# Performance work log

Measured on AMD Instinct MI355X. Metric: run time of the kernel, lower is better.

## Reference

```python
import jax, jax.numpy as jnp
import numpy as np

B, E, F = 16384, 128, 6
ITEM_V, CATE_V, HIST = 91718, 11, 50
I_IDX, J_IDX = np.triu_indices(F, k=1)  # 15 field pairs, loop order (0,1),(0,2),...
EPS = 1e-5


def _xavier(key, shape):
    fan_in, fan_out = shape[0], shape[-1]
    std = (2.0 / (fan_in + fan_out)) ** 0.5
    return std * jax.random.normal(key, shape, dtype=jnp.float32)


def setup_inputs() -> dict:
    key = jax.random.key(0)
    ks = jax.random.split(key, 20)
    inp = {
        'item_id': jax.random.randint(ks[0], (B,), 0, ITEM_V),
        'item_emb_d128': jax.random.normal(ks[1], (B, 128), dtype=jnp.float32),
        'likes_level': jax.random.randint(ks[2], (B,), 0, CATE_V),
        'views_level': jax.random.randint(ks[3], (B,), 0, CATE_V),
        'item_seq': jax.random.randint(ks[4], (B, HIST), 0, ITEM_V),
        # learned parameters
        'item_emb': 0.05 * jax.random.normal(ks[5], (ITEM_V, E), dtype=jnp.float32),
        'cate_emb': 0.05 * jax.random.normal(ks[6], (CATE_V, E), dtype=jnp.float32),
        'mm_W': _xavier(ks[7], (128, E)), 'mm_b': jnp.zeros((E,), jnp.float32),
        'ln_g': jnp.ones((E,), jnp.float32), 'ln_b': jnp.zeros((E,), jnp.float32),
        'se_W1': _xavier(ks[8], (F, F // 2)), 'se_b1': jnp.zeros((F // 2,), jnp.float32),
        'se_W2': _xavier(ks[9], (F // 2, F)), 'se_b2': jnp.zeros((F,), jnp.float32),
        'bi_W': _xavier(ks[10], (E, E)),
        'mlp_W1': _xavier(ks[11], (21 * E, 512)), 'mlp_b1': jnp.zeros((512,), jnp.float32),
        'bn1_g': jnp.ones((512,), jnp.float32), 'bn1_b': jnp.zeros((512,), jnp.float32),
        'bn1_rm': jnp.zeros((512,), jnp.float32), 'bn1_rv': jnp.ones((512,), jnp.float32),
        'mlp_W2': _xavier(ks[12], (512, 256)), 'mlp_b2': jnp.zeros((256,), jnp.float32),
        'bn2_g': jnp.ones((256,), jnp.float32), 'bn2_b': jnp.zeros((256,), jnp.float32),
        'bn2_rm': jnp.zeros((256,), jnp.float32), 'bn2_rv': jnp.ones((256,), jnp.float32),
        'mlp_W3': _xavier(ks[13], (256, 1)), 'mlp_b3': jnp.zeros((1,), jnp.float32),
    }
    return inp


def _forward(item_id, item_emb_d128, likes_level, views_level, item_seq,
             item_emb, cate_emb, mm_W, mm_b, ln_g, ln_b,
             se_W1, se_b1, se_W2, se_b2, bi_W,
             mlp_W1, mlp_b1, bn1_g, bn1_b, bn1_rm, bn1_rv,
             mlp_W2, mlp_b2, bn2_g, bn2_b, bn2_rm, bn2_rv,
             mlp_W3, mlp_b3):
    b = item_id.shape[0]
    tab = item_emb.at[0].set(0.0)  # padding_idx=0
    like_feat = cate_emb[likes_level]
    view_feat = cate_emb[views_level]
    item_feat = tab[item_id]
    # mm_proj: Linear -> LayerNorm -> ReLU
    mm = item_emb_d128 @ mm_W + mm_b
    mu = mm.mean(-1, keepdims=True)
    var = jnp.var(mm, axis=-1, keepdims=True)
    mm = jax.nn.relu((mm - mu) / jnp.sqrt(var + EPS) * ln_g + ln_b)
    # masked mean pooling over history
    seq_emb = tab[item_seq]                               # (B, HIST, E)
    valid = (item_seq != 0).astype(seq_emb.dtype)
    seq_sum = (seq_emb * valid[..., None]).sum(1)
    cnt = jnp.clip(valid.sum(1, keepdims=True), 1.0)
    hist_feat = seq_sum / cnt
    user_feat = jnp.zeros((b, E), seq_emb.dtype)
    x = jnp.stack([user_feat, like_feat, view_feat, item_feat, mm, hist_feat], axis=1)  # (B,6,E)
    # SENet
    z = x.mean(-1)
    w = jax.nn.sigmoid(jax.nn.relu(z @ se_W1 + se_b1) @ se_W2 + se_b2)
    xs = x * w[:, :, None]
    # bilinear 'all'
    xw = jnp.einsum('bfe,ed->bfd', xs, bi_W)
    p = xs[:, I_IDX, :] * xw[:, J_IDX, :]                 # (B,15,E)
    c = jnp.concatenate([xs.reshape(b, -1), p.reshape(b, -1)], axis=1)  # (B, 2688)
    # MLP head (eval mode: BN uses running stats, dropout off)
    h = c @ mlp_W1 + mlp_b1
    h = jax.nn.relu((h - bn1_rm) / jnp.sqrt(bn1_rv + EPS) * bn1_g + bn1_b)
    h = h @ mlp_W2 + mlp_b2
    h = jax.nn.relu((h - bn2_rm) / jnp.sqrt(bn2_rv + EPS) * bn2_g + bn2_b)
    logits = h @ mlp_W3 + mlp_b3
    return jax.nn.sigmoid(logits)[:, 0]


def reference(item_id, item_emb_d128, likes_level, views_level, item_seq,
              item_emb, cate_emb, mm_W, mm_b, ln_g, ln_b,
              se_W1, se_b1, se_W2, se_b2, bi_W,
              mlp_W1, mlp_b1, bn1_g, bn1_b, bn1_rm, bn1_rv,
              mlp_W2, mlp_b2, bn2_g, bn2_b, bn2_rm, bn2_rv,
              mlp_W3, mlp_b3):
    return _forward(item_id, item_emb_d128, likes_level, views_level, item_seq,
                    item_emb, cate_emb, mm_W, mm_b, ln_g, ln_b,
                    se_W1, se_b1, se_W2, se_b2, bi_W,
                    mlp_W1, mlp_b1, bn1_g, bn1_b, bn1_rm, bn1_rv,
                    mlp_W2, mlp_b2, bn2_g, bn2_b, bn2_rm, bn2_rv,
                    mlp_W3, mlp_b3)
```

## Files before the change

kernel.cpp:

```cpp
#include <hip/hip_runtime.h>
#include <hip/hip_bf16.h>

typedef __hip_bfloat16 bfloat;
typedef __bf16 bf16x8 __attribute__((ext_vector_type(8)));
typedef float f32x4 __attribute__((ext_vector_type(4)));

#define B_SZ   16384
#define E_DIM  128
#define HIST_L 50


__device__ __constant__ int ISL[10] = {0,0,0,0,1,1,1,2,2,3};

__device__ __forceinline__ void gl_lds16(const void* g, void* l) {
    __builtin_amdgcn_global_load_lds(
        (const __attribute__((address_space(1))) unsigned int*)g,
        (__attribute__((address_space(3))) unsigned int*)l, 16, 0, 0);
}

template<int TB>
__global__ __launch_bounds__(256) void feat_kernel(
    const int* __restrict__ item_id,
    const int* __restrict__ likes, const int* __restrict__ views,
    const int* __restrict__ seq,
    const void* __restrict__ item_tab, const float* __restrict__ cate_emb,
    const float* __restrict__ mm,
    const float* __restrict__ ln_g, const float* __restrict__ ln_b,
    const float* __restrict__ se_W1, const float* __restrict__ se_b1,
    const float* __restrict__ se_W2, const float* __restrict__ se_b2,
    bfloat* __restrict__ xs)
{
    const int tid = threadIdx.x;
    const int r   = tid >> 7;
    const int e   = tid & 127;
    const int b   = blockIdx.x * 2 + r;
    const int w   = tid >> 6;

    __shared__ float redh[2][4][128];
    __shared__ int   seq_s[2][64];
    __shared__ float lnred[4], lnred2[4];
    __shared__ float zred[5][4];
    __shared__ float wsh[2][6];
    __shared__ int   cnt_s[2];

    if (e < 64) seq_s[r][e] = (e < HIST_L) ? seq[(size_t)b * HIST_L + e] : 0;
    __syncthreads();

    const int iid = item_id[b];
    const float like_v = cate_emb[likes[b] * 128 + e];
    const float view_v = cate_emb[views[b] * 128 + e];
    float item_v;
    if (TB) {
        const bfloat* tb = (const bfloat*)item_tab;
        item_v = __bfloat162float(tb[(size_t)iid * 128 + e]);
    } else {
        const float* tf = (const float*)item_tab;
        float raw = tf[(size_t)iid * 128 + e];
        item_v = iid ? raw : 0.f;
    }
    const float acc = mm[(size_t)b * 128 + e];

    const int q   = e >> 5;
    const int l32 = e & 31;
    float4 hs = make_float4(0.f, 0.f, 0.f, 0.f);
    if (TB) {
        const ushort* tb = (const ushort*)item_tab;
        #pragma unroll
        for (int g = 0; g < 13; ++g) {
            int s = seq_s[r][g * 4 + q];
            ushort4 v = *(const ushort4*)&tb[(size_t)s * 128 + l32 * 4];
            hs.x += __bfloat162float(__ushort_as_bfloat16(v.x));
            hs.y += __bfloat162float(__ushort_as_bfloat16(v.y));
            hs.z += __bfloat162float(__ushort_as_bfloat16(v.z));
            hs.w += __bfloat162float(__ushort_as_bfloat16(v.w));
        }
    } else {
        const float* tf = (const float*)item_tab;
        #pragma unroll
        for (int g = 0; g < 13; ++g) {
            int s = seq_s[r][g * 4 + q];
            const float4 v = *(const float4*)&tf[(size_t)s * 128 + l32 * 4];
            float m = (s != 0) ? 1.f : 0.f;
            hs.x = fmaf(v.x, m, hs.x);
            hs.y = fmaf(v.y, m, hs.y);
            hs.z = fmaf(v.z, m, hs.z);
            hs.w = fmaf(v.w, m, hs.w);
        }
    }

    {
        float v = acc;
        #pragma unroll
        for (int off = 32; off > 0; off >>= 1) v += __shfl_down(v, off, 64);
        if ((tid & 63) == 0) lnred[w] = v;
    }
    __syncthreads();
    const float mu = (lnred[2 * r] + lnred[2 * r + 1]) * (1.f / 128.f);
    const float d  = acc - mu;
    {
        float v = d * d;
        #pragma unroll
        for (int off = 32; off > 0; off >>= 1) v += __shfl_down(v, off, 64);
        if ((tid & 63) == 0) lnred2[w] = v;
    }
    redh[r][q][l32 * 4 + 0] = hs.x;
    redh[r][q][l32 * 4 + 1] = hs.y;
    redh[r][q][l32 * 4 + 2] = hs.z;
    redh[r][q][l32 * 4 + 3] = hs.w;
    if ((w & 1) == 0 && e < 64) {
        bool valid = (e < HIST_L) && (seq_s[r][e] != 0);
        unsigned long long m = __ballot(valid);
        if (e == 0) cnt_s[r] = (int)__popcll(m);
    }
    __syncthreads();
    const float var = (lnred2[2 * r] + lnred2[2 * r + 1]) * (1.f / 128.f);
    float xmm = d * rsqrtf(var + 1e-5f) * ln_g[e] + ln_b[e];
    xmm = fmaxf(xmm, 0.f);

    const int cnt = cnt_s[r] > 0 ? cnt_s[r] : 1;
    const float hist_v = (redh[r][0][e] + redh[r][1][e] +
                          redh[r][2][e] + redh[r][3][e]) / (float)cnt;

    {
        float s1 = like_v, s2 = view_v, s3 = item_v, s4 = xmm, s5 = hist_v;
        #pragma unroll
        for (int off = 32; off > 0; off >>= 1) {
            s1 += __shfl_down(s1, off, 64);
            s2 += __shfl_down(s2, off, 64);
            s3 += __shfl_down(s3, off, 64);
            s4 += __shfl_down(s4, off, 64);
            s5 += __shfl_down(s5, off, 64);
        }
        if ((tid & 63) == 0) {
            zred[0][w] = s1; zred[1][w] = s2; zred[2][w] = s3;
            zred[3][w] = s4; zred[4][w] = s5;
        }
    }
    __syncthreads();

    if (e == 0) {
        float z[6];
        z[0] = 0.f;
        #pragma unroll
        for (int f = 1; f < 6; ++f)
            z[f] = (zred[f - 1][2 * r] + zred[f - 1][2 * r + 1]) * (1.f / 128.f);
        float a[3];
        #pragma unroll
        for (int j = 0; j < 3; ++j) {
            float s = se_b1[j];
            #pragma unroll
            for (int f = 0; f < 6; ++f) s += z[f] * se_W1[f * 3 + j];
            a[j] = fmaxf(s, 0.f);
        }
        #pragma unroll
        for (int f = 0; f < 6; ++f) {
            float s = se_b2[f];
            #pragma unroll
            for (int j = 0; j < 3; ++j) s += a[j] * se_W2[j * 6 + f];
            wsh[r][f] = 1.f / (1.f + expf(-s));
        }
    }
    __syncthreads();

    bfloat* xrow = xs + (size_t)b * 640;
    xrow[0 * 128 + e] = __float2bfloat16(like_v * wsh[r][1]);
    xrow[1 * 128 + e] = __float2bfloat16(view_v * wsh[r][2]);
    xrow[2 * 128 + e] = __float2bfloat16(item_v * wsh[r][3]);
    xrow[3 * 128 + e] = __float2bfloat16(xmm    * wsh[r][4]);
    xrow[4 * 128 + e] = __float2bfloat16(hist_v * wsh[r][5]);
}

__global__ __launch_bounds__(256) void transpose_W1c(
    const float* __restrict__ W1, bfloat* __restrict__ W1t)
{
    __shared__ float t[64][65];
    const int tid = threadIdx.x;
    const int kk0 = blockIdx.x * 64, n0 = blockIdx.y * 64;
    const int j = tid & 63;
    #pragma unroll
    for (int p = 0; p < 16; ++p) {
        int i = (tid >> 6) + p * 4;
        int kk = kk0 + i;
        int orig = kk + (kk < 640 ? 128 : 768);
        t[i][j] = W1[(size_t)orig * 512 + n0 + j];
    }
    __syncthreads();
    #pragma unroll
    for (int p = 0; p < 16; ++p) {
        int i = (tid >> 6) + p * 4;
        W1t[(size_t)(n0 + i) * 1920 + kk0 + j] = __float2bfloat16(t[j][i]);
    }
}

__global__ __launch_bounds__(256) void prep_kernel(
    const float* __restrict__ W2, const float* __restrict__ bi_W,
    const float* __restrict__ mm_W,
    bfloat* __restrict__ W2t, bfloat* __restrict__ bWt,
    bfloat* __restrict__ mmWt,
    const float* __restrict__ lb1, const float* __restrict__ g1,
    const float* __restrict__ bb1, const float* __restrict__ rm1,
    const float* __restrict__ rv1,
    const float* __restrict__ lb2, const float* __restrict__ g2,
    const float* __restrict__ bb2, const float* __restrict__ rm2,
    const float* __restrict__ rv2,
    const float* __restrict__ mm_b,
    float* __restrict__ S1, float* __restrict__ T1,
    float* __restrict__ S2, float* __restrict__ T2,
    float* __restrict__ Tmm)
{
    int idx = blockIdx.x * 256 + threadIdx.x;
    if (idx < 131072) {
        int k = idx >> 8, n = idx & 255;
        W2t[(size_t)n * 512 + k] = __float2bfloat16(W2[idx]);
    } else if (idx < 147456) {
        int t = idx - 131072;
        int k = t >> 7, n = t & 127;
        bWt[n * 128 + k] = __float2bfloat16(bi_W[t]);
    } else if (idx < 163840) {
        int t = idx - 147456;
        int k = t >> 7, n = t & 127;
        mmWt[n * 128 + k] = __float2bfloat16(mm_W[t]);
    } else if (idx < 164352) {
        int j = idx - 163840;
        float s = g1[j] * rsqrtf(rv1[j] + 1e-5f);
        S1[j] = s;
        T1[j] = (lb1[j] - rm1[j]) * s + bb1[j];
    } else if (idx < 164608) {
        int j = idx - 164352;
        float s = g2[j] * rsqrtf(rv2[j] + 1e-5f);
        S2[j] = s;
        T2[j] = (lb2[j] - rm2[j]) * s + bb2[j];
    } else if (idx < 164736) {
        int j = idx - 164608;
        Tmm[j] = mm_b[j];
    }
}

__global__ __launch_bounds__(256) void cvt_emb(
    const float* __restrict__ in, bfloat* __restrict__ out, int n8)
{
    int idx = blockIdx.x * 256 + threadIdx.x;
    if (idx >= n8) return;
    if (idx < 16) {
        union { bf16x8 v; unsigned short s[8]; } z;
        #pragma unroll
        for (int i = 0; i < 8; ++i) z.s[i] = 0;
        ((bf16x8*)out)[idx] = z.v;
        return;
    }
    float4 f0 = ((const float4*)in)[idx * 2];
    float4 f1 = ((const float4*)in)[idx * 2 + 1];
    union { bf16x8 v; unsigned short s[8]; } u;
    u.s[0] = __bfloat16_as_ushort(__float2bfloat16(f0.x));
    u.s[1] = __bfloat16_as_ushort(__float2bfloat16(f0.y));
    u.s[2] = __bfloat16_as_ushort(__float2bfloat16(f0.z));
    u.s[3] = __bfloat16_as_ushort(__float2bfloat16(f0.w));
    u.s[4] = __bfloat16_as_ushort(__float2bfloat16(f1.x));
    u.s[5] = __bfloat16_as_ushort(__float2bfloat16(f1.y));
    u.s[6] = __bfloat16_as_ushort(__float2bfloat16(f1.z));
    u.s[7] = __bfloat16_as_ushort(__float2bfloat16(f1.w));
    ((bf16x8*)out)[idx] = u.v;
}

template<int MODE, int EPI, int F32OUT>
__global__ __launch_bounds__(256, 2) void gemm_bt(
    const void* __restrict__ A, const bfloat* __restrict__ A2,
    const bfloat* __restrict__ Bt, void* __restrict__ C,
    int M, int N, int K,
    const float* __restrict__ S, const float* __restrict__ T)
{
    __shared__ __align__(16) short As[4][128 * 32];
    __shared__ __align__(16) short Bs[4][128 * 32];

    const int tid  = threadIdx.x;
    const int bm   = blockIdx.x * 128;
    const int bn   = blockIdx.y * 128;
    const int wave = tid >> 6;
    const int lane = tid & 63;
    const int wm   = (wave >> 1) * 64;
    const int wn   = (wave & 1) * 64;

    const short* Ag  = (const short*)A;
    const short* A2g = (const short*)A2;
    const short* Bg  = (const short*)Bt;

    f32x4 acc[4][4];
    #pragma unroll
    for (int i = 0; i < 4; ++i)
        #pragma unroll
        for (int j = 0; j < 4; ++j)
            acc[i][j] = (f32x4){0.f, 0.f, 0.f, 0.f};

    const int srow = tid >> 2;
    const int sck  = tid & 3;

    auto stage = [&](int buf, int kt) {
        #pragma unroll
        for (int rr = 0; rr < 2; ++rr) {
            int row = srow + rr * 64;
            int g   = sck ^ ((row >> 1) & 3);
            gl_lds16(&Bg[(long)(bn + row) * K + kt + g * 8],
                     &Bs[buf][row * 32 + sck * 8]);
        }
        if (MODE == 3) {
            const float* Af = (const float*)A;
            #pragma unroll
            for (int rr = 0; rr < 2; ++rr) {
                int row = srow + rr * 64;
                int g   = sck ^ ((row >> 1) & 3);
                long aoff = (long)(bm + row) * K + kt + g * 8;
                float4 f0 = *(const float4*)&Af[aoff];
                float4 f1 = *(const float4*)&Af[aoff + 4];
                union { bf16x8 v; unsigned short s[8]; } u;
                u.s[0] = __bfloat16_as_ushort(__float2bfloat16(f0.x));
                u.s[1] = __bfloat16_as_ushort(__float2bfloat16(f0.y));
                u.s[2] = __bfloat16_as_ushort(__float2bfloat16(f0.z));
                u.s[3] = __bfloat16_as_ushort(__float2bfloat16(f0.w));
                u.s[4] = __bfloat16_as_ushort(__float2bfloat16(f1.x));
                u.s[5] = __bfloat16_as_ushort(__float2bfloat16(f1.y));
                u.s[6] = __bfloat16_as_ushort(__float2bfloat16(f1.z));
                u.s[7] = __bfloat16_as_ushort(__float2bfloat16(f1.w));
                *(bf16x8*)&As[buf][row * 32 + sck * 8] = u.v;
            }
        } else {
            #pragma unroll
            for (int rr = 0; rr < 2; ++rr) {
                int row = srow + rr * 64;
                int g   = sck ^ ((row >> 1) & 3);
                const short* src;
                if (MODE == 4) {
                    long rb = (long)(bm + row);
                    src = (kt < 640)
                        ? &Ag [rb * 640  + kt + g * 8]
                        : &A2g[rb * 1280 + (kt - 640) + g * 8];
                } else if (MODE == 2) {
                    int gr = bm + row;
                    src = &Ag[((long)(gr >> 2)) * 640 +
                              ((gr & 3) + 1) * 128 + kt + g * 8];
                } else {
                    src = &Ag[(long)(bm + row) * K + kt + g * 8];
                }
                gl_lds16(src, &As[buf][row * 32 + sck * 8]);
            }
        }
    };

    const int rbase = lane & 15;
    const int cg    = lane >> 4;
    const int ca    = (cg ^ ((rbase >> 1) & 3)) << 3;

    const int nk = K >> 5;
    stage(0, 0);
    stage(1, 32);
    if (nk > 2) stage(2, 64);

    for (int i = 0; i < nk; ++i) {
        if (MODE == 3)
            asm volatile("s_waitcnt vmcnt(0) lgkmcnt(0)" ::: "memory");
        else if (i + 2 < nk)
            asm volatile("s_waitcnt vmcnt(8)" ::: "memory");
        else if (i + 1 < nk)
            asm volatile("s_waitcnt vmcnt(4)" ::: "memory");
        else
            asm volatile("s_waitcnt vmcnt(0)" ::: "memory");
        __builtin_amdgcn_s_barrier();
        __builtin_amdgcn_sched_barrier(0);

        const int cur = i & 3;
        bf16x8 af[4], bfr[4];
        #pragma unroll
        for (int mt = 0; mt < 4; ++mt)
            af[mt] = *(const bf16x8*)
                &As[cur][(wm + mt * 16 + rbase) * 32 + ca];
        #pragma unroll
        for (int nt = 0; nt < 4; ++nt)
            bfr[nt] = *(const bf16x8*)
                &Bs[cur][(wn + nt * 16 + rbase) * 32 + ca];
        #pragma unroll
        for (int mt = 0; mt < 4; ++mt)
            #pragma unroll
            for (int nt = 0; nt < 4; ++nt)
                acc[mt][nt] = __builtin_amdgcn_mfma_f32_16x16x32_bf16(
                    af[mt], bfr[nt], acc[mt][nt], 0, 0, 0);

        if (i + 3 < nk) stage((i + 3) & 3, (i + 3) << 5);
    }

    const int col0 = lane & 15;
    const int row0 = (lane >> 4) * 4;
    #pragma unroll
    for (int nt = 0; nt < 4; ++nt) {
        int col = bn + wn + nt * 16 + col0;
        float s = 1.f, t = 0.f;
        if (EPI == 1 || EPI == 2) { s = (EPI == 1) ? S[col] : 1.f; t = T[col]; }
        #pragma unroll
        for (int mt = 0; mt < 4; ++mt) {
            #pragma unroll
            for (int i = 0; i < 4; ++i) {
                int row = bm + wm + mt * 16 + row0 + i;
                float v = acc[mt][nt][i];
                if (EPI == 3) {
                    const bfloat* xsp = (const bfloat*)A;
                    bfloat* Pp = (bfloat*)C;
                    long b = row >> 2;
                    int pplist[4];
                    int npp;
                    if (i == 0)      { npp = 1; pplist[0] = 0; }
                    else if (i == 1) { npp = 2; pplist[0] = 1; pplist[1] = 4; }
                    else if (i == 2) { npp = 3; pplist[0] = 2; pplist[1] = 5; pplist[2] = 7; }
                    else             { npp = 4; pplist[0] = 3; pplist[1] = 6; pplist[2] = 8; pplist[3] = 9; }
                    #pragma unroll
                    for (int t2 = 0; t2 < npp; ++t2) {
                        int pp  = pplist[t2];
                        int isl = ISL[pp];
                        float xv = __bfloat162float(
                            xsp[b * 640 + isl * 128 + col]);
                        Pp[b * 1280 + pp * 128 + col] =
                            __float2bfloat16(xv * v);
                    }
                } else {
                    if (EPI == 1) v = fmaxf(v * s + t, 0.f);
                    if (EPI == 2) v = v + t;
                    if (F32OUT) ((float*)C)[(size_t)row * N + col] = v;
                    else ((bfloat*)C)[(size_t)row * N + col] = __float2bfloat16(v);
                }
            }
        }
    }
}

__global__ __launch_bounds__(256) void head_kernel(
    const bfloat* __restrict__ h2, const float* __restrict__ W3,
    const float* __restrict__ b3, float* __restrict__ out)
{
    int lane = threadIdx.x & 63;
    int row  = blockIdx.x * 4 + (threadIdx.x >> 6);
    float acc = 0.f;
    #pragma unroll
    for (int i = 0; i < 4; ++i)
        acc += __bfloat162float(h2[(size_t)row * 256 + i * 64 + lane]) *
               W3[i * 64 + lane];
    #pragma unroll
    for (int off = 32; off > 0; off >>= 1) acc += __shfl_down(acc, off, 64);
    if (lane == 0) {
        float l = acc + b3[0];
        out[row] = 1.f / (1.f + expf(-l));
    }
}

extern "C" void kernel_launch(void* const* d_in, const int* in_sizes, int n_in,
                              void* d_out, int out_size, void* d_ws, size_t ws_size,
                              hipStream_t stream) {
    const int*   item_id = (const int*)  d_in[0];
    const float* d128    = (const float*)d_in[1];
    const int*   likes   = (const int*)  d_in[2];
    const int*   views   = (const int*)  d_in[3];
    const int*   seq     = (const int*)  d_in[4];
    const float* item_emb= (const float*)d_in[5];
    const float* cate_emb= (const float*)d_in[6];
    const float* mm_W    = (const float*)d_in[7];
    const float* mm_b    = (const float*)d_in[8];
    const float* ln_g    = (const float*)d_in[9];
    const float* ln_b    = (const float*)d_in[10];
    const float* se_W1   = (const float*)d_in[11];
    const float* se_b1   = (const float*)d_in[12];
    const float* se_W2   = (const float*)d_in[13];
    const float* se_b2   = (const float*)d_in[14];
    const float* bi_W    = (const float*)d_in[15];
    const float* W1      = (const float*)d_in[16];
    const float* b1      = (const float*)d_in[17];
    const float* bn1_g   = (const float*)d_in[18];
    const float* bn1_b   = (const float*)d_in[19];
    const float* bn1_rm  = (const float*)d_in[20];
    const float* bn1_rv  = (const float*)d_in[21];
    const float* W2      = (const float*)d_in[22];
    const float* b2      = (const float*)d_in[23];
    const float* bn2_g   = (const float*)d_in[24];
    const float* bn2_b   = (const float*)d_in[25];
    const float* bn2_rm  = (const float*)d_in[26];
    const float* bn2_rv  = (const float*)d_in[27];
    const float* W3      = (const float*)d_in[28];
    const float* b3      = (const float*)d_in[29];

    const size_t fixed = 2300416;
    const size_t ITB   = 23479808;
    int CH; bool use_tb;
    if      (fixed + ITB + (size_t)16384 * 4864 <= ws_size) { CH = 16384; use_tb = true;  }
    else if (fixed + (size_t)16384 * 4864 <= ws_size)       { CH = 16384; use_tb = false; }
    else if (fixed + ITB + (size_t)8192 * 4864 <= ws_size)  { CH = 8192;  use_tb = true;  }
    else if (fixed + (size_t)8192 * 4864 <= ws_size)        { CH = 8192;  use_tb = false; }
    else if (fixed + ITB + (size_t)4096 * 4864 <= ws_size)  { CH = 4096;  use_tb = true;  }
    else if (fixed + (size_t)4096 * 4864 <= ws_size)        { CH = 4096;  use_tb = false; }
    else if (fixed + (size_t)2048 * 4864 <= ws_size)        { CH = 2048;  use_tb = false; }
    else                                                    { CH = 1024;  use_tb = false; }

    char* ws = (char*)d_ws;
    bfloat* W1t = (bfloat*)(ws);
    bfloat* W2t = (bfloat*)(ws + 1966080);
    bfloat* bWt = (bfloat*)(ws + 2228224);
    bfloat* mmWt= (bfloat*)(ws + 2260992);
    float*  S1  = (float*) (ws + 2293760);
    float*  T1  = (float*) (ws + 2295808);
    float*  S2  = (float*) (ws + 2297856);
    float*  T2  = (float*) (ws + 2298880);
    float*  Tmm = (float*) (ws + 2299904);
    bfloat* itemb = (bfloat*)(ws + fixed);
    char*   cb  = ws + fixed + (use_tb ? ITB : 0);
    bfloat* xs  = (bfloat*)(cb);
    bfloat* h1  = (bfloat*)(cb + (size_t)CH * 1280);
    bfloat* P   = (bfloat*)(cb + (size_t)CH * 2304);
    float*  mm  = (float*)P;
    bfloat* h2  = (bfloat*)P;

    transpose_W1c<<<dim3(30, 8), 256, 0, stream>>>(W1, W1t);
    prep_kernel<<<(164736 + 255) / 256, 256, 0, stream>>>(
        W2, bi_W, mm_W, W2t, bWt, mmWt,
        b1, bn1_g, bn1_b, bn1_rm, bn1_rv,
        b2, bn2_g, bn2_b, bn2_rm, bn2_rv,
        mm_b, S1, T1, S2, T2, Tmm);
    if (use_tb) {
        const int n8 = 91718 * 128 / 8;
        cvt_emb<<<(n8 + 255) / 256, 256, 0, stream>>>(item_emb, itemb, n8);
    }

    for (int off = 0; off < B_SZ; off += CH) {
        dim3 gmm(CH / 128, 1);
        gemm_bt<3, 2, 1><<<gmm, 256, 0, stream>>>(
            d128 + (size_t)off * 128, nullptr, mmWt, mm,
            CH, 128, 128, nullptr, Tmm);

        if (use_tb)
            feat_kernel<1><<<CH / 2, 256, 0, stream>>>(
                item_id + off, likes + off, views + off,
                seq + (size_t)off * HIST_L, itemb, cate_emb, mm,
                ln_g, ln_b, se_W1, se_b1, se_W2, se_b2, xs);
        else
            feat_kernel<0><<<CH / 2, 256, 0, stream>>>(
                item_id + off, likes + off, views + off,
                seq + (size_t)off * HIST_L, item_emb, cate_emb, mm,
                ln_g, ln_b, se_W1, se_b1, se_W2, se_b2, xs);

        dim3 gxw(CH * 4 / 128, 1);
        gemm_bt<2, 3, 0><<<gxw, 256, 0, stream>>>(
            xs, nullptr, bWt, P, CH * 4, 128, 128, nullptr, nullptr);

        dim3 g1(CH / 128, 4);
        gemm_bt<4, 1, 0><<<g1, 256, 0, stream>>>(
            xs, P, W1t, h1, CH, 512, 1920, S1, T1);

        dim3 g2(CH / 128, 2);
        gemm_bt<0, 1, 0><<<g2, 256, 0, stream>>>(
            h1, nullptr, W2t, h2, CH, 256, 512, S2, T2);

        head_kernel<<<CH / 4, 256, 0, stream>>>(h2, W3, b3, (float*)d_out + off);
    }
}
```

Baseline: 276.3 us.

## Add dedicated 256x128 triple-buffered GEMM kernel for MLP layer one

Replaces the generic 128x128 tile GEMM for the first MLP layer with a specialized kernel that uses 256x128 tiles, K-steps of 64, a three-stage LDS pipeline in 144KB of dynamic shared memory, and an XOR swizzle layout. Each wave computes a 128x64 sub-tile, so each loaded operand feeds more MFMAs and global and LDS traffic per flop drops. In exchange occupancy falls to one block per CU, the grid has half as many blocks, and the accumulators take far more registers.

```diff
diff --git a/kernel.cpp b/kernel.cpp
--- a/kernel.cpp
+++ b/kernel.cpp
@@ -262,6 +262,115 @@
     ((bf16x8*)out)[idx] = u.v;
 }
 
+__global__ __launch_bounds__(256, 1) void gemm_mlp1(
+    const bfloat* __restrict__ Axs, const bfloat* __restrict__ Ap,
+    const bfloat* __restrict__ Bt, bfloat* __restrict__ C,
+    int M, int N, int K,
+    const float* __restrict__ S, const float* __restrict__ T)
+{
+    extern __shared__ __align__(16) short smem[];
+
+    const int tid  = threadIdx.x;
+    const int bm   = blockIdx.x * 256;
+    const int bn   = blockIdx.y * 128;
+    const int wave = tid >> 6;
+    const int lane = tid & 63;
+    const int wm   = (wave >> 1) * 128;
+    const int wn   = (wave & 1) * 64;
+
+    const short* Ag  = (const short*)Axs;
+    const short* A2g = (const short*)Ap;
+    const short* Bg  = (const short*)Bt;
+
+    f32x4 acc[8][4];
+    #pragma unroll
+    for (int i = 0; i < 8; ++i)
+        #pragma unroll
+        for (int j = 0; j < 4; ++j)
+            acc[i][j] = (f32x4){0.f, 0.f, 0.f, 0.f};
+
+    const int l8  = lane >> 3;
+    const int gch = (lane & 7) ^ l8;
+
+    auto stage = [&](int buf, int kt) {
+        short* Ab = smem + buf * 24576;
+        short* Bb = Ab + 16384;
+        #pragma unroll
+        for (int d = 0; d < 4; ++d) {
+            int seg = wave * 4 + d;
+            int row = seg * 8 + l8;
+            gl_lds16(&Bg[(long)(bn + row) * K + kt + gch * 8],
+                     &Bb[seg * 512 + lane * 8]);
+        }
+        #pragma unroll
+        for (int d = 0; d < 8; ++d) {
+            int seg = wave * 8 + d;
+            int row = seg * 8 + l8;
+            long rb = (long)(bm + row);
+            const short* src = (kt < 640)
+                ? &Ag [rb * 640  + kt + gch * 8]
+                : &A2g[rb * 1280 + (kt - 640) + gch * 8];
+            gl_lds16(src, &Ab[seg * 512 + lane * 8]);
+        }
+    };
+
+    const int rbase = lane & 15;
+    const int rsw   = rbase & 7;
+
+    const int nk = K >> 6;
+    stage(0, 0);
+    stage(1, 64);
+
+    for (int i = 0; i < nk; ++i) {
+        if (i + 1 < nk) asm volatile("s_waitcnt vmcnt(12)" ::: "memory");
+        else            asm volatile("s_waitcnt vmcnt(0)" ::: "memory");
+        __builtin_amdgcn_s_barrier();
+        __builtin_amdgcn_sched_barrier(0);
+
+        if (i + 2 < nk) stage((i + 2) % 3, (i + 2) << 6);
+
+        const short* Ab = smem + (i % 3) * 24576;
+        const short* Bb = Ab + 16384;
+        #pragma unroll
+        for (int h = 0; h < 2; ++h) {
+            const int cg = h * 4 + (lane >> 4);
+            const int ca = (cg ^ rsw) << 3;
+            bf16x8 af[8], bfr[4];
+            #pragma unroll
+            for (int mt = 0; mt < 8; ++mt)
+                af[mt] = *(const bf16x8*)
+                    &Ab[(wm + mt * 16 + rbase) * 64 + ca];
+            #pragma unroll
+            for (int nt = 0; nt < 4; ++nt)
+                bfr[nt] = *(const bf16x8*)
+                    &Bb[(wn + nt * 16 + rbase) * 64 + ca];
+            #pragma unroll
+            for (int mt = 0; mt < 8; ++mt)
+                #pragma unroll
+                for (int nt = 0; nt < 4; ++nt)
+                    acc[mt][nt] = __builtin_amdgcn_mfma_f32_16x16x32_bf16(
+                        af[mt], bfr[nt], acc[mt][nt], 0, 0, 0);
+        }
+    }
+
+    const int col0 = lane & 15;
+    const int row0 = (lane >> 4) * 4;
+    #pragma unroll
+    for (int nt = 0; nt < 4; ++nt) {
+        int col = bn + wn + nt * 16 + col0;
+        float s = S[col], t = T[col];
+        #pragma unroll
+        for (int mt = 0; mt < 8; ++mt) {
+            #pragma unroll
+            for (int i = 0; i < 4; ++i) {
+                int row = bm + wm + mt * 16 + row0 + i;
+                float v = fmaxf(acc[mt][nt][i] * s + t, 0.f);
+                C[(size_t)row * N + col] = __float2bfloat16(v);
+            }
+        }
+    }
+}
+
 template<int MODE, int EPI, int F32OUT>
 __global__ __launch_bounds__(256, 2) void gemm_bt(
     const void* __restrict__ A, const bfloat* __restrict__ A2,
@@ -328,12 +437,7 @@
                 int row = srow + rr * 64;
                 int g   = sck ^ ((row >> 1) & 3);
                 const short* src;
-                if (MODE == 4) {
-                    long rb = (long)(bm + row);
-                    src = (kt < 640)
-                        ? &Ag [rb * 640  + kt + g * 8]
-                        : &A2g[rb * 1280 + (kt - 640) + g * 8];
-                } else if (MODE == 2) {
+                if (MODE == 2) {
                     int gr = bm + row;
                     src = &Ag[((long)(gr >> 2)) * 640 +
                               ((gr & 3) + 1) * 128 + kt + g * 8];
@@ -544,8 +648,8 @@
         gemm_bt<2, 3, 0><<<gxw, 256, 0, stream>>>(
             xs, nullptr, bWt, P, CH * 4, 128, 128, nullptr, nullptr);
 
-        dim3 g1(CH / 128, 4);
-        gemm_bt<4, 1, 0><<<g1, 256, 0, stream>>>(
+        dim3 g1(CH / 256, 4);
+        gemm_mlp1<<<g1, 256, 147456, stream>>>(
             xs, P, W1t, h1, CH, 512, 1920, S1, T1);
 
         dim3 g2(CH / 128, 2);
```

Result: no change. 278.1 us (+0.7%).

## Merge prep kernels into one launch and pre-convert d128 to bf16

Applied to the files above, without the earlier changes.

Merges the W1 transpose, the small weight prep, and the item-embedding bf16 conversion into one mega_prep kernel that dispatches on block index, and adds a pass converting item_emb_d128 to bf16 in a new workspace region. The mm projection GEMM then takes bf16 input through the async global-to-LDS path instead of converting fp32 inline with a full wait every k-step. This cuts launch count and lets the first GEMM pipeline its loads, at the cost of an extra 4 MB write and read and a larger workspace requirement that could push the chunk size down.

```diff
diff --git a/kernel.cpp b/kernel.cpp
--- a/kernel.cpp
+++ b/kernel.cpp
@@ -170,29 +170,8 @@
     xrow[4 * 128 + e] = __float2bfloat16(hist_v * wsh[r][5]);
 }
 
-__global__ __launch_bounds__(256) void transpose_W1c(
-    const float* __restrict__ W1, bfloat* __restrict__ W1t)
-{
-    __shared__ float t[64][65];
-    const int tid = threadIdx.x;
-    const int kk0 = blockIdx.x * 64, n0 = blockIdx.y * 64;
-    const int j = tid & 63;
-    #pragma unroll
-    for (int p = 0; p < 16; ++p) {
-        int i = (tid >> 6) + p * 4;
-        int kk = kk0 + i;
-        int orig = kk + (kk < 640 ? 128 : 768);
-        t[i][j] = W1[(size_t)orig * 512 + n0 + j];
-    }
-    __syncthreads();
-    #pragma unroll
-    for (int p = 0; p < 16; ++p) {
-        int i = (tid >> 6) + p * 4;
-        W1t[(size_t)(n0 + i) * 1920 + kk0 + j] = __float2bfloat16(t[j][i]);
-    }
-}
-
-__global__ __launch_bounds__(256) void prep_kernel(
+__global__ __launch_bounds__(256) void mega_prep(
+    const float* __restrict__ W1, bfloat* __restrict__ W1t,
     const float* __restrict__ W2, const float* __restrict__ bi_W,
     const float* __restrict__ mm_W,
     bfloat* __restrict__ W2t, bfloat* __restrict__ bWt,
@@ -206,60 +185,94 @@
     const float* __restrict__ mm_b,
     float* __restrict__ S1, float* __restrict__ T1,
     float* __restrict__ S2, float* __restrict__ T2,
-    float* __restrict__ Tmm)
+    float* __restrict__ Tmm,
+    const float* __restrict__ d128, bfloat* __restrict__ d128b,
+    const float* __restrict__ item_emb, bfloat* __restrict__ itemb)
 {
-    int idx = blockIdx.x * 256 + threadIdx.x;
-    if (idx < 131072) {
-        int k = idx >> 8, n = idx & 255;
-        W2t[(size_t)n * 512 + k] = __float2bfloat16(W2[idx]);
-    } else if (idx < 147456) {
-        int t = idx - 131072;
-        int k = t >> 7, n = t & 127;
-        bWt[n * 128 + k] = __float2bfloat16(bi_W[t]);
-    } else if (idx < 163840) {
-        int t = idx - 147456;
-        int k = t >> 7, n = t & 127;
-        mmWt[n * 128 + k] = __float2bfloat16(mm_W[t]);
-    } else if (idx < 164352) {
-        int j = idx - 163840;
-        float s = g1[j] * rsqrtf(rv1[j] + 1e-5f);
-        S1[j] = s;
-        T1[j] = (lb1[j] - rm1[j]) * s + bb1[j];
-    } else if (idx < 164608) {
-        int j = idx - 164352;
-        float s = g2[j] * rsqrtf(rv2[j] + 1e-5f);
-        S2[j] = s;
-        T2[j] = (lb2[j] - rm2[j]) * s + bb2[j];
-    } else if (idx < 164736) {
-        int j = idx - 164608;
-        Tmm[j] = mm_b[j];
-    }
-}
-
-__global__ __launch_bounds__(256) void cvt_emb(
-    const float* __restrict__ in, bfloat* __restrict__ out, int n8)
-{
-    int idx = blockIdx.x * 256 + threadIdx.x;
-    if (idx >= n8) return;
-    if (idx < 16) {
-        union { bf16x8 v; unsigned short s[8]; } z;
-        #pragma unroll
-        for (int i = 0; i < 8; ++i) z.s[i] = 0;
-        ((bf16x8*)out)[idx] = z.v;
-        return;
-    }
-    float4 f0 = ((const float4*)in)[idx * 2];
-    float4 f1 = ((const float4*)in)[idx * 2 + 1];
-    union { bf16x8 v; unsigned short s[8]; } u;
-    u.s[0] = __bfloat16_as_ushort(__float2bfloat16(f0.x));
-    u.s[1] = __bfloat16_as_ushort(__float2bfloat16(f0.y));
-    u.s[2] = __bfloat16_as_ushort(__float2bfloat16(f0.z));
-    u.s[3] = __bfloat16_as_ushort(__float2bfloat16(f0.w));
-    u.s[4] = __bfloat16_as_ushort(__float2bfloat16(f1.x));
-    u.s[5] = __bfloat16_as_ushort(__float2bfloat16(f1.y));
-    u.s[6] = __bfloat16_as_ushort(__float2bfloat16(f1.z));
-    u.s[7] = __bfloat16_as_ushort(__float2bfloat16(f1.w));
-    ((bf16x8*)out)[idx] = u.v;
+    const int blk = blockIdx.x;
+    const int tid = threadIdx.x;
+    if (blk < 240) {
+        __shared__ float t[64][65];
+        const int kk0 = (blk % 30) * 64, n0 = (blk / 30) * 64;
+        const int j = tid & 63;
+        #pragma unroll
+        for (int p = 0; p < 16; ++p) {
+            int i = (tid >> 6) + p * 4;
+            int kk = kk0 + i;
+            int orig = kk + (kk < 640 ? 128 : 768);
+            t[i][j] = W1[(size_t)orig * 512 + n0 + j];
+        }
+        __syncthreads();
+        #pragma unroll
+        for (int p = 0; p < 16; ++p) {
+            int i = (tid >> 6) + p * 4;
+            W1t[(size_t)(n0 + i) * 1920 + kk0 + j] = __float2bfloat16(t[j][i]);
+        }
+    } else if (blk < 884) {
+        int idx = (blk - 240) * 256 + tid;
+        if (idx < 131072) {
+            int k = idx >> 8, n = idx & 255;
+            W2t[(size_t)n * 512 + k] = __float2bfloat16(W2[idx]);
+        } else if (idx < 147456) {
+            int t2 = idx - 131072;
+            int k = t2 >> 7, n = t2 & 127;
+            bWt[n * 128 + k] = __float2bfloat16(bi_W[t2]);
+        } else if (idx < 163840) {
+            int t2 = idx - 147456;
+            int k = t2 >> 7, n = t2 & 127;
+            mmWt[n * 128 + k] = __float2bfloat16(mm_W[t2]);
+        } else if (idx < 164352) {
+            int j = idx - 163840;
+            float s = g1[j] * rsqrtf(rv1[j] + 1e-5f);
+            S1[j] = s;
+            T1[j] = (lb1[j] - rm1[j]) * s + bb1[j];
+        } else if (idx < 164608) {
+            int j = idx - 164352;
+            float s = g2[j] * rsqrtf(rv2[j] + 1e-5f);
+            S2[j] = s;
+            T2[j] = (lb2[j] - rm2[j]) * s + bb2[j];
+        } else if (idx < 164736) {
+            Tmm[idx - 164608] = mm_b[idx - 164608];
+        }
+    } else if (blk < 1908) {
+        int idx = (blk - 884) * 256 + tid;
+        float4 f0 = ((const float4*)d128)[idx * 2];
+        float4 f1 = ((const float4*)d128)[idx * 2 + 1];
+        union { bf16x8 v; unsigned short s[8]; } u;
+        u.s[0] = __bfloat16_as_ushort(__float2bfloat16(f0.x));
+        u.s[1] = __bfloat16_as_ushort(__float2bfloat16(f0.y));
+        u.s[2] = __bfloat16_as_ushort(__float2bfloat16(f0.z));
+        u.s[3] = __bfloat16_as_ushort(__float2bfloat16(f0.w));
+        u.s[4] = __bfloat16_as_ushort(__float2bfloat16(f1.x));
+        u.s[5] = __bfloat16_as_ushort(__float2bfloat16(f1.y));
+        u.s[6] = __bfloat16_as_ushort(__float2bfloat16(f1.z));
+        u.s[7] = __bfloat16_as_ushort(__float2bfloat16(f1.w));
+        ((bf16x8*)d128b)[idx] = u.v;
+    } else {
+        if (itemb == nullptr) return;
+        const int n8 = 91718 * 128 / 8;
+        int idx = (blk - 1908) * 256 + tid;
+        if (idx >= n8) return;
+        if (idx < 16) {
+            union { bf16x8 v; unsigned short s[8]; } z;
+            #pragma unroll
+            for (int i = 0; i < 8; ++i) z.s[i] = 0;
+            ((bf16x8*)itemb)[idx] = z.v;
+            return;
+        }
+        float4 f0 = ((const float4*)item_emb)[idx * 2];
+        float4 f1 = ((const float4*)item_emb)[idx * 2 + 1];
+        union { bf16x8 v; unsigned short s[8]; } u;
+        u.s[0] = __bfloat16_as_ushort(__float2bfloat16(f0.x));
+        u.s[1] = __bfloat16_as_ushort(__float2bfloat16(f0.y));
+        u.s[2] = __bfloat16_as_ushort(__float2bfloat16(f0.z));
+        u.s[3] = __bfloat16_as_ushort(__float2bfloat16(f0.w));
+        u.s[4] = __bfloat16_as_ushort(__float2bfloat16(f1.x));
+        u.s[5] = __bfloat16_as_ushort(__float2bfloat16(f1.y));
+        u.s[6] = __bfloat16_as_ushort(__float2bfloat16(f1.z));
+        u.s[7] = __bfloat16_as_ushort(__float2bfloat16(f1.w));
+        ((bf16x8*)itemb)[idx] = u.v;
+    }
 }
 
 template<int MODE, int EPI, int F32OUT>
@@ -302,46 +315,24 @@
             gl_lds16(&Bg[(long)(bn + row) * K + kt + g * 8],
                      &Bs[buf][row * 32 + sck * 8]);
         }
-        if (MODE == 3) {
-            const float* Af = (const float*)A;
-            #pragma unroll
-            for (int rr = 0; rr < 2; ++rr) {
-                int row = srow + rr * 64;
-                int g   = sck ^ ((row >> 1) & 3);
-                long aoff = (long)(bm + row) * K + kt + g * 8;
-                float4 f0 = *(const float4*)&Af[aoff];
-                float4 f1 = *(const float4*)&Af[aoff + 4];
-                union { bf16x8 v; unsigned short s[8]; } u;
-                u.s[0] = __bfloat16_as_ushort(__float2bfloat16(f0.x));
-                u.s[1] = __bfloat16_as_ushort(__float2bfloat16(f0.y));
-                u.s[2] = __bfloat16_as_ushort(__float2bfloat16(f0.z));
-                u.s[3] = __bfloat16_as_ushort(__float2bfloat16(f0.w));
-                u.s[4] = __bfloat16_as_ushort(__float2bfloat16(f1.x));
-                u.s[5] = __bfloat16_as_ushort(__float2bfloat16(f1.y));
-                u.s[6] = __bfloat16_as_ushort(__float2bfloat16(f1.z));
-                u.s[7] = __bfloat16_as_ushort(__float2bfloat16(f1.w));
-                *(bf16x8*)&As[buf][row * 32 + sck * 8] = u.v;
+        #pragma unroll
+        for (int rr = 0; rr < 2; ++rr) {
+            int row = srow + rr * 64;
+            int g   = sck ^ ((row >> 1) & 3);
+            const short* src;
+            if (MODE == 4) {
+                long rb = (long)(bm + row);
+                src = (kt < 640)
+                    ? &Ag [rb * 640  + kt + g * 8]
+                    : &A2g[rb * 1280 + (kt - 640) + g * 8];
+            } else if (MODE == 2) {
+                int gr = bm + row;
+                src = &Ag[((long)(gr >> 2)) * 640 +
+                          ((gr & 3) + 1) * 128 + kt + g * 8];
+            } else {
+                src = &Ag[(long)(bm + row) * K + kt + g * 8];
             }
-        } else {
-            #pragma unroll
-            for (int rr = 0; rr < 2; ++rr) {
-                int row = srow + rr * 64;
-                int g   = sck ^ ((row >> 1) & 3);
-                const short* src;
-                if (MODE == 4) {
-                    long rb = (long)(bm + row);
-                    src = (kt < 640)
-                        ? &Ag [rb * 640  + kt + g * 8]
-                        : &A2g[rb * 1280 + (kt - 640) + g * 8];
-                } else if (MODE == 2) {
-                    int gr = bm + row;
-                    src = &Ag[((long)(gr >> 2)) * 640 +
-                              ((gr & 3) + 1) * 128 + kt + g * 8];
-                } else {
-                    src = &Ag[(long)(bm + row) * K + kt + g * 8];
-                }
-                gl_lds16(src, &As[buf][row * 32 + sck * 8]);
-            }
+            gl_lds16(src, &As[buf][row * 32 + sck * 8]);
         }
     };
 
@@ -355,9 +346,7 @@
     if (nk > 2) stage(2, 64);
 
     for (int i = 0; i < nk; ++i) {
-        if (MODE == 3)
-            asm volatile("s_waitcnt vmcnt(0) lgkmcnt(0)" ::: "memory");
-        else if (i + 2 < nk)
+        if (i + 2 < nk)
             asm volatile("s_waitcnt vmcnt(8)" ::: "memory");
         else if (i + 1 < nk)
             asm volatile("s_waitcnt vmcnt(4)" ::: "memory");
@@ -483,16 +472,17 @@
     const float* b3      = (const float*)d_in[29];
 
     const size_t fixed = 2300416;
+    const size_t DB    = 4194304;
     const size_t ITB   = 23479808;
     int CH; bool use_tb;
-    if      (fixed + ITB + (size_t)16384 * 4864 <= ws_size) { CH = 16384; use_tb = true;  }
-    else if (fixed + (size_t)16384 * 4864 <= ws_size)       { CH = 16384; use_tb = false; }
-    else if (fixed + ITB + (size_t)8192 * 4864 <= ws_size)  { CH = 8192;  use_tb = true;  }
-    else if (fixed + (size_t)8192 * 4864 <= ws_size)        { CH = 8192;  use_tb = false; }
-    else if (fixed + ITB + (size_t)4096 * 4864 <= ws_size)  { CH = 4096;  use_tb = true;  }
-    else if (fixed + (size_t)4096 * 4864 <= ws_size)        { CH = 4096;  use_tb = false; }
-    else if (fixed + (size_t)2048 * 4864 <= ws_size)        { CH = 2048;  use_tb = false; }
-    else                                                    { CH = 1024;  use_tb = false; }
+    if      (fixed + DB + ITB + (size_t)16384 * 4864 <= ws_size) { CH = 16384; use_tb = true;  }
+    else if (fixed + DB + (size_t)16384 * 4864 <= ws_size)       { CH = 16384; use_tb = false; }
+    else if (fixed + DB + ITB + (size_t)8192 * 4864 <= ws_size)  { CH = 8192;  use_tb = true;  }
+    else if (fixed + DB + (size_t)8192 * 4864 <= ws_size)        { CH = 8192;  use_tb = false; }
+    else if (fixed + DB + ITB + (size_t)4096 * 4864 <= ws_size)  { CH = 4096;  use_tb = true;  }
+    else if (fixed + DB + (size_t)4096 * 4864 <= ws_size)        { CH = 4096;  use_tb = false; }
+    else if (fixed + DB + (size_t)2048 * 4864 <= ws_size)        { CH = 2048;  use_tb = false; }
+    else                                                         { CH = 1024;  use_tb = false; }
 
     char* ws = (char*)d_ws;
     bfloat* W1t = (bfloat*)(ws);
@@ -504,29 +494,30 @@
     float*  S2  = (float*) (ws + 2297856);
     float*  T2  = (float*) (ws + 2298880);
     float*  Tmm = (float*) (ws + 2299904);
-    bfloat* itemb = (bfloat*)(ws + fixed);
-    char*   cb  = ws + fixed + (use_tb ? ITB : 0);
+    bfloat* d128b = (bfloat*)(ws + fixed);
+    bfloat* itemb = (bfloat*)(ws + fixed + DB);
+    char*   cb  = ws + fixed + DB + (use_tb ? ITB : 0);
     bfloat* xs  = (bfloat*)(cb);
     bfloat* h1  = (bfloat*)(cb + (size_t)CH * 1280);
     bfloat* P   = (bfloat*)(cb + (size_t)CH * 2304);
     float*  mm  = (float*)P;
     bfloat* h2  = (bfloat*)P;
 
-    transpose_W1c<<<dim3(30, 8), 256, 0, stream>>>(W1, W1t);
-    prep_kernel<<<(164736 + 255) / 256, 256, 0, stream>>>(
-        W2, bi_W, mm_W, W2t, bWt, mmWt,
-        b1, bn1_g, bn1_b, bn1_rm, bn1_rv,
-        b2, bn2_g, bn2_b, bn2_rm, bn2_rv,
-        mm_b, S1, T1, S2, T2, Tmm);
-    if (use_tb) {
-        const int n8 = 91718 * 128 / 8;
-        cvt_emb<<<(n8 + 255) / 256, 256, 0, stream>>>(item_emb, itemb, n8);
+    {
+        int nblk = 1908 + (use_tb ? (91718 * 128 / 8 + 255) / 256 : 0);
+        mega_prep<<<nblk, 256, 0, stream>>>(
+            W1, W1t, W2, bi_W, mm_W, W2t, bWt, mmWt,
+            b1, bn1_g, bn1_b, bn1_rm, bn1_rv,
+            b2, bn2_g, bn2_b, bn2_rm, bn2_rv,
+            mm_b, S1, T1, S2, T2, Tmm,
+            d128, d128b,
+            item_emb, use_tb ? itemb : nullptr);
     }
 
     for (int off = 0; off < B_SZ; off += CH) {
         dim3 gmm(CH / 128, 1);
-        gemm_bt<3, 2, 1><<<gmm, 256, 0, stream>>>(
-            d128 + (size_t)off * 128, nullptr, mmWt, mm,
+        gemm_bt<0, 2, 1><<<gmm, 256, 0, stream>>>(
+            d128b + (size_t)off * 128, nullptr, mmWt, mm,
             CH, 128, 128, nullptr, Tmm);
 
         if (use_tb)
```

Result: no change. 271.8 us (-1.6%).
